# Performance work log

Measured on AMD Instinct MI355X. Metric: run time of the kernel, lower is better.

The kernel has to match this reference:

```python
import jax, jax.numpy as jnp
import numpy as np


def _maxpool2(x):
    # 2x2 max pool, stride 2, valid padding (H, W even). x: [B,H,W,C]
    B, H, W, C = x.shape
    return x.reshape(B, H // 2, 2, W // 2, 2, C).max(axis=(2, 4))


def setup_inputs() -> dict:
    key = jax.random.key(0)
    ks = jax.random.split(key, 9)
    B, H, W, C = 8, 64, 64, 512
    cfg, ch = C // 8, C // 2
    std = 0.02
    return {
        "x": jax.random.normal(ks[0], (B, H, W, C), jnp.float32),
        "theta_w": jax.random.normal(ks[1], (C, cfg), jnp.float32) * std,
        "theta_b": jnp.zeros((cfg,), jnp.float32),
        "phi_w": jax.random.normal(ks[2], (C, cfg), jnp.float32) * std,
        "phi_b": jnp.zeros((cfg,), jnp.float32),
        "g_w": jax.random.normal(ks[3], (C, ch), jnp.float32) * std,
        "g_b": jnp.zeros((ch,), jnp.float32),
        "o3_w": jax.random.normal(ks[4], (ch, C), jnp.float32) * std,
        "o3_b": jnp.zeros((C,), jnp.float32),
        # original initializes gamma to 0; use 0.1 so the attention branch contributes
        "gamma": jnp.full((1,), 0.1, jnp.float32),
    }


def reference(x, theta_w, theta_b, phi_w, phi_b, g_w, g_b, o3_w, o3_b, gamma):
    B, H, W, C = x.shape
    cfg = theta_w.shape[1]
    ch = g_w.shape[1]
    hw = H * W
    hwd = (H // 2) * (W // 2)

    theta = jnp.einsum("bhwc,cf->bhwf", x, theta_w) + theta_b          # [B,H,W,cfg]
    phi = _maxpool2(jnp.einsum("bhwc,cf->bhwf", x, phi_w) + phi_b)     # [B,H/2,W/2,cfg]
    g = _maxpool2(jnp.einsum("bhwc,cg->bhwg", x, g_w) + g_b)           # [B,H/2,W/2,ch]

    theta_f = theta.reshape(B, hw, cfg)
    phi_f = phi.reshape(B, hwd, cfg)
    g_f = g.reshape(B, hwd, ch)

    # s[b,i,j] = phi[b,i] . theta[b,j]; softmax over j (last axis, Keras default)
    s = jnp.einsum("bif,bjf->bij", phi_f, theta_f)                     # [B,hwd,hw]
    beta = jax.nn.softmax(s, axis=-1)
    # o = matmul(beta, g, transpose_a=True): o[b,j,c] = sum_i beta[b,i,j] g[b,i,c]
    o = jnp.einsum("bij,bic->bjc", beta, g_f)                          # [B,hw,ch]
    o = o.reshape(B, H, W, ch)
    o = jnp.einsum("bhwg,gc->bhwc", o, o3_w) + o3_b                    # [B,H,W,C]
    return gamma * o + x
```

## Files before the change

### kernel.cpp

```cpp
#include <hip/hip_runtime.h>
#include <cstdint>

typedef short short8 __attribute__((ext_vector_type(8)));
typedef float floatx4 __attribute__((ext_vector_type(4)));

__device__ __forceinline__ unsigned short f2bf(float f) {
    unsigned int u = __builtin_bit_cast(unsigned int, f);
    u += 0x7FFFu + ((u >> 16) & 1u);
    return (unsigned short)(u >> 16);
}
__device__ __forceinline__ float bf2f(unsigned short h) {
    unsigned int u = ((unsigned int)h) << 16;
    return __builtin_bit_cast(float, u);
}

__device__ __forceinline__ void async_copy16(const void* g, void* lds) {
    __builtin_amdgcn_global_load_lds(
        (const __attribute__((address_space(1))) void*)g,
        (__attribute__((address_space(3))) void*)lds, 16, 0, 0);
}

__device__ __forceinline__ int swz(int row, int koff) {
    return koff ^ (((row >> 2) & 3) << 4);
}

template<bool AFP32, int EPI>
__global__ __launch_bounds__(256) void mfma_gemm(
    const void* __restrict__ Avoid, const unsigned short* __restrict__ B,
    void* __restrict__ Cout, const float* __restrict__ bias,
    const float* __restrict__ gamma, const float* __restrict__ resid,
    int lda, int ldb, int ldc, int K)
{
    __shared__ unsigned short As[4096];
    __shared__ unsigned short Bs[4096];

    const int tid = threadIdx.x;
    const int wv = tid >> 6, ln = tid & 63;
    const int r16 = ln & 15, q8 = ln >> 4;
    const int wm = (wv >> 1) * 64, wn = (wv & 1) * 64;
    const int m0 = blockIdx.y * 128, n0 = blockIdx.x * 128;

    floatx4 acc[4][4] = {};

    for (int k0 = 0; k0 < K; k0 += 32) {
        if (AFP32) {
            const float* Af = (const float*)Avoid;
            #pragma unroll
            for (int p = 0; p < 4; ++p) {
                int u = p * 256 + tid;
                int row = u >> 3, c4 = u & 7;
                float4 v = *(const float4*)(Af + (size_t)(m0 + row) * lda + k0 + c4 * 4);
                ushort4 h;
                h.x = f2bf(v.x); h.y = f2bf(v.y); h.z = f2bf(v.z); h.w = f2bf(v.w);
                *(ushort4*)&As[row * 32 + c4 * 4] = h;
            }
            #pragma unroll
            for (int q = 0; q < 2; ++q) {
                int chunk = wv * 2 + q;
                int e = (chunk << 9) + ln * 8;
                int row = e >> 5, col = e & 31;
                async_copy16(B + (size_t)(n0 + row) * ldb + (k0 + col), &Bs[chunk << 9]);
            }
        } else {
            const unsigned short* Ag = (const unsigned short*)Avoid;
            #pragma unroll
            for (int q = 0; q < 2; ++q) {
                int chunk = wv * 2 + q;
                int e = (chunk << 9) + ln * 8;
                int row = e >> 5, col = e & 31;
                async_copy16(Ag + (size_t)(m0 + row) * lda + (k0 + col), &As[chunk << 9]);
                async_copy16(B + (size_t)(n0 + row) * ldb + (k0 + col), &Bs[chunk << 9]);
            }
        }
        __syncthreads();

        short8 af[4], bff[4];
        #pragma unroll
        for (int i = 0; i < 4; ++i) {
            af[i]  = *(const short8*)&As[(wm + i * 16 + r16) * 32 + q8 * 8];
            bff[i] = *(const short8*)&Bs[(wn + i * 16 + r16) * 32 + q8 * 8];
        }
        #pragma unroll
        for (int mi = 0; mi < 4; ++mi)
            #pragma unroll
            for (int ni = 0; ni < 4; ++ni)
                acc[mi][ni] = __builtin_amdgcn_mfma_f32_16x16x32_bf16(
                    af[mi], bff[ni], acc[mi][ni], 0, 0, 0);
        __syncthreads();
    }

    if (EPI == 2) {
        float* C = (float*)Cout;
        const float gm = gamma[0];
        #pragma unroll
        for (int ni = 0; ni < 4; ++ni) {
            const int n = n0 + wn + ni * 16 + r16;
            const float bs = bias[n];
            #pragma unroll
            for (int mi = 0; mi < 4; ++mi)
                #pragma unroll
                for (int r = 0; r < 4; ++r) {
                    int m = m0 + wm + mi * 16 + q8 * 4 + r;
                    C[(size_t)m * ldc + n] = gm * (acc[mi][ni][r] + bs) + resid[(size_t)m * ldc + n];
                }
        }
    } else {
        unsigned short* C = (unsigned short*)Cout;
        #pragma unroll
        for (int ni = 0; ni < 4; ++ni) {
            const int n = n0 + wn + ni * 16 + r16;
            const float bs = bias[n];
            #pragma unroll
            for (int mi = 0; mi < 4; ++mi)
                #pragma unroll
                for (int r = 0; r < 4; ++r) {
                    int m = m0 + wm + mi * 16 + q8 * 4 + r;
                    C[(size_t)m * ldc + n] = f2bf(acc[mi][ni][r] + bs);
                }
        }
    }
}

__global__ __launch_bounds__(256) void phase1_l_kernel(
    const unsigned short* __restrict__ tpgF,
    const unsigned short* __restrict__ phiP,
    float* __restrict__ lbuf)
{
    __shared__ unsigned short th_s[8192];
    __shared__ unsigned short ph_s[4096];
    const int tid = threadIdx.x, wv = tid >> 6, ln = tid & 63;
    const int r16 = ln & 15, q8 = ln >> 4, lsub = ln >> 3, l8 = ln & 7;
    const int jsp = blockIdx.x, i0 = blockIdx.y * 64, b = blockIdx.z;

    #pragma unroll
    for (int q = 0; q < 2; ++q) {
        int chunk = wv * 2 + q, row = chunk * 8 + lsub;
        int so = swz(row, l8 * 8);
        async_copy16(phiP + (size_t)(b * 1024 + i0 + row) * 64 + so, &ph_s[chunk * 512]);
    }

    float colsum[4] = {0.f, 0.f, 0.f, 0.f};
    for (int jc = 0; jc < 8; ++jc) {
        const int j0 = jsp * 1024 + jc * 128;
        __syncthreads();
        #pragma unroll
        for (int q = 0; q < 4; ++q) {
            int chunk = wv * 4 + q, row = chunk * 8 + lsub;
            int so = swz(row, l8 * 8);
            async_copy16(tpgF + (size_t)(b * 4096 + j0 + row) * 384 + so, &th_s[chunk * 512]);
        }
        __syncthreads();

        floatx4 sacc[2][4] = {};
        #pragma unroll
        for (int ks = 0; ks < 2; ++ks) {
            short8 af[2], bf[4];
            #pragma unroll
            for (int mi = 0; mi < 2; ++mi)
                af[mi] = *(const short8*)&th_s[(wv * 32 + mi * 16 + r16) * 64 + swz(r16, ks * 32 + q8 * 8)];
            #pragma unroll
            for (int ni = 0; ni < 4; ++ni)
                bf[ni] = *(const short8*)&ph_s[(ni * 16 + r16) * 64 + swz(r16, ks * 32 + q8 * 8)];
            #pragma unroll
            for (int mi = 0; mi < 2; ++mi)
                #pragma unroll
                for (int ni = 0; ni < 4; ++ni)
                    sacc[mi][ni] = __builtin_amdgcn_mfma_f32_16x16x32_bf16(
                        af[mi], bf[ni], sacc[mi][ni], 0, 0, 0);
        }
        #pragma unroll
        for (int mi = 0; mi < 2; ++mi)
            #pragma unroll
            for (int ni = 0; ni < 4; ++ni)
                #pragma unroll
                for (int r = 0; r < 4; ++r)
                    colsum[ni] += __expf(sacc[mi][ni][r] - 20.f);
    }
    #pragma unroll
    for (int ni = 0; ni < 4; ++ni) {
        float s = colsum[ni];
        s += __shfl_xor(s, 16);
        s += __shfl_xor(s, 32);
        if (q8 == 0) atomicAdd(&lbuf[b * 1024 + i0 + ni * 16 + r16], s);
    }
}

__global__ __launch_bounds__(512) void attn_fused_kernel(
    const unsigned short* __restrict__ tpgF,
    const unsigned short* __restrict__ phiP,
    const unsigned short* __restrict__ gPT,
    unsigned short* __restrict__ o_)
{
    __shared__ unsigned short th_es[8192];
    __shared__ unsigned short ph_s[2][4096];
    __shared__ unsigned short gs[2][16384];

    const int tid = threadIdx.x, wv = tid >> 6, ln = tid & 63;
    const int r16 = ln & 15, q8 = ln >> 4, lsub = ln >> 3, l8 = ln & 7;
    const int j0 = blockIdx.x * 128, b = blockIdx.y;
    const int jh = wv >> 2, it = wv & 3;

    #pragma unroll
    for (int q = 0; q < 2; ++q) {
        int chunk = wv * 2 + q, row = chunk * 8 + lsub;
        async_copy16(tpgF + (size_t)(b * 4096 + j0 + row) * 384 + swz(row, l8 * 8),
                     &th_es[chunk * 512]);
    }
    {
        int row = wv * 8 + lsub;
        async_copy16(phiP + (size_t)(b * 1024 + row) * 64 + swz(row, l8 * 8),
                     &ph_s[0][wv * 512]);
        #pragma unroll
        for (int q = 0; q < 4; ++q) {
            int chunk = wv * 4 + q, c = chunk * 8 + lsub;
            async_copy16(gPT + (size_t)(b * 256 + c) * 1024 + swz(c, l8 * 8),
                         &gs[0][chunk * 512]);
        }
    }
    asm volatile("s_waitcnt vmcnt(5)" ::: "memory");
    __builtin_amdgcn_sched_barrier(0);
    __builtin_amdgcn_s_barrier();
    __builtin_amdgcn_sched_barrier(0);

    short8 thf[4][2];
    #pragma unroll
    for (int mi = 0; mi < 4; ++mi)
        #pragma unroll
        for (int ks = 0; ks < 2; ++ks)
            thf[mi][ks] = *(const short8*)&th_es[(jh * 64 + mi * 16 + r16) * 64
                                                 + swz(r16, ks * 32 + q8 * 8)];
    asm volatile("s_waitcnt lgkmcnt(0)" ::: "memory");
    __builtin_amdgcn_sched_barrier(0);

    floatx4 acc[4][4] = {};

    for (int t = 0; t < 16; ++t) {
        const int buf = t & 1, nbuf = buf ^ 1;
        if (t < 15) {
            const int i0n = (t + 1) * 64;
            int row = wv * 8 + lsub;
            async_copy16(phiP + (size_t)(b * 1024 + i0n + row) * 64 + swz(row, l8 * 8),
                         &ph_s[nbuf][wv * 512]);
            #pragma unroll
            for (int q = 0; q < 4; ++q) {
                int chunk = wv * 4 + q, c = chunk * 8 + lsub;
                async_copy16(gPT + (size_t)(b * 256 + c) * 1024 + i0n + swz(c, l8 * 8),
                             &gs[nbuf][chunk * 512]);
            }
            asm volatile("s_waitcnt vmcnt(5)" ::: "memory");
        } else {
            asm volatile("s_waitcnt vmcnt(0)" ::: "memory");
        }
        __builtin_amdgcn_sched_barrier(0);
        __builtin_amdgcn_s_barrier();
        __builtin_amdgcn_sched_barrier(0);

        floatx4 sacc[4] = {};
        #pragma unroll
        for (int ks = 0; ks < 2; ++ks) {
            short8 pf = *(const short8*)&ph_s[buf][(it * 16 + r16) * 64
                                                   + swz(r16, ks * 32 + q8 * 8)];
            #pragma unroll
            for (int mi = 0; mi < 4; ++mi)
                sacc[mi] = __builtin_amdgcn_mfma_f32_16x16x32_bf16(
                    thf[mi][ks], pf, sacc[mi], 0, 0, 0);
        }
        #pragma unroll
        for (int mi = 0; mi < 4; ++mi)
            #pragma unroll
            for (int r = 0; r < 4; ++r) {
                int j = jh * 64 + mi * 16 + q8 * 4 + r;
                th_es[j * 64 + (((it ^ q8) << 4) | r16)] = f2bf(__expf(sacc[mi][r] - 20.f));
            }
        asm volatile("s_waitcnt lgkmcnt(0)" ::: "memory");
        __builtin_amdgcn_sched_barrier(0);
        __builtin_amdgcn_s_barrier();
        __builtin_amdgcn_sched_barrier(0);

        #pragma unroll
        for (int ks = 0; ks < 2; ++ks) {
            short8 ef[4], gf[4];
            #pragma unroll
            for (int mi = 0; mi < 4; ++mi)
                ef[mi] = *(const short8*)&th_es[(jh * 64 + mi * 16 + r16) * 64
                                                + swz(r16, ks * 32 + q8 * 8)];
            #pragma unroll
            for (int ni = 0; ni < 4; ++ni)
                gf[ni] = *(const short8*)&gs[buf][(it * 64 + ni * 16 + r16) * 64
                                                  + swz(r16, ks * 32 + q8 * 8)];
            #pragma unroll
            for (int mi = 0; mi < 4; ++mi)
                #pragma unroll
                for (int ni = 0; ni < 4; ++ni)
                    acc[mi][ni] = __builtin_amdgcn_mfma_f32_16x16x32_bf16(
                        ef[mi], gf[ni], acc[mi][ni], 0, 0, 0);
        }
        asm volatile("s_waitcnt lgkmcnt(0)" ::: "memory");
        __builtin_amdgcn_sched_barrier(0);
        __builtin_amdgcn_s_barrier();
        __builtin_amdgcn_sched_barrier(0);
    }

    #pragma unroll
    for (int mi = 0; mi < 4; ++mi)
        #pragma unroll
        for (int ni = 0; ni < 4; ++ni)
            #pragma unroll
            for (int r = 0; r < 4; ++r) {
                int j = j0 + jh * 64 + mi * 16 + q8 * 4 + r;
                int c = it * 64 + ni * 16 + r16;
                o_[((size_t)b * 4096 + j) * 256 + c] = f2bf(acc[mi][ni][r]);
            }
}

__global__ __launch_bounds__(256) void prep_w_kernel(
    const float* __restrict__ theta_w, const float* __restrict__ phi_w,
    const float* __restrict__ g_w, const float* __restrict__ o3_w,
    const float* __restrict__ theta_b, const float* __restrict__ phi_b,
    const float* __restrict__ g_b,
    unsigned short* __restrict__ tpgwT, unsigned short* __restrict__ o3wT,
    float* __restrict__ biasTPG, float* __restrict__ lbuf)
{
    int t = blockIdx.x * 256 + threadIdx.x;
    if (t < 196608) {
        int n = t >> 9, k = t & 511;
        float v = (n < 64) ? theta_w[k * 64 + n]
                : (n < 128) ? phi_w[k * 64 + (n - 64)]
                : g_w[k * 256 + (n - 128)];
        tpgwT[t] = f2bf(v);
    } else if (t < 327680) {
        int e = t - 196608; int n = e >> 8, k = e & 255;
        o3wT[e] = f2bf(o3_w[k * 512 + n]);
    } else if (t < 328064) {
        int j = t - 327680;
        biasTPG[j] = (j < 64) ? theta_b[j] : (j < 128) ? phi_b[j - 64] : g_b[j - 128];
    } else if (t < 336256) {
        lbuf[t - 328064] = 0.f;
    }
}

__global__ __launch_bounds__(256) void maxpool_phi_kernel(
    const unsigned short* __restrict__ tpgF, unsigned short* __restrict__ phiP)
{
    int t = blockIdx.x * 256 + threadIdx.x;
    int f = t & 63, i = (t >> 6) & 1023, b = t >> 16;
    int ph = i >> 5, pw = i & 31;
    size_t base = ((size_t)(b * 64 + 2 * ph) * 64 + 2 * pw) * 384 + 64 + f;
    float v0 = bf2f(tpgF[base]),         v1 = bf2f(tpgF[base + 384]);
    float v2 = bf2f(tpgF[base + 24576]), v3 = bf2f(tpgF[base + 24576 + 384]);
    phiP[t] = f2bf(fmaxf(fmaxf(v0, v1), fmaxf(v2, v3)));
}

__global__ __launch_bounds__(256) void maxpoolT_g_kernel(
    const unsigned short* __restrict__ tpgF, const float* __restrict__ lbuf,
    unsigned short* __restrict__ gPT)
{
    __shared__ unsigned short tile[16][256];
    __shared__ float rls[16];
    int b = blockIdx.y, i0 = blockIdx.x * 16, c = threadIdx.x;
    if (c < 16) rls[c] = 1.0f / lbuf[b * 1024 + i0 + c];
    __syncthreads();
    #pragma unroll
    for (int il = 0; il < 16; ++il) {
        int i = i0 + il, ph = i >> 5, pw = i & 31;
        size_t base = ((size_t)(b * 64 + 2 * ph) * 64 + 2 * pw) * 384 + 128 + c;
        float v0 = bf2f(tpgF[base]),         v1 = bf2f(tpgF[base + 384]);
        float v2 = bf2f(tpgF[base + 24576]), v3 = bf2f(tpgF[base + 24576 + 384]);
        tile[il][c] = f2bf(fmaxf(fmaxf(v0, v1), fmaxf(v2, v3)) * rls[il]);
    }
    __syncthreads();
    unsigned short* dst = gPT + ((size_t)(b * 256 + c) * 1024 + i0);
    short8 v0, v1;
    #pragma unroll
    for (int il = 0; il < 8; ++il) { v0[il] = (short)tile[il][c]; v1[il] = (short)tile[il + 8][c]; }
    *(short8*)dst = v0;
    *(short8*)(dst + 8) = v1;
}

extern "C" void kernel_launch(void* const* d_in, const int* in_sizes, int n_in,
                              void* d_out, int out_size, void* d_ws, size_t ws_size,
                              hipStream_t stream)
{
    const float* x       = (const float*)d_in[0];
    const float* theta_w = (const float*)d_in[1];
    const float* theta_b = (const float*)d_in[2];
    const float* phi_w   = (const float*)d_in[3];
    const float* phi_b   = (const float*)d_in[4];
    const float* g_w     = (const float*)d_in[5];
    const float* g_b     = (const float*)d_in[6];
    const float* o3_w    = (const float*)d_in[7];
    const float* o3_b    = (const float*)d_in[8];
    const float* gamma   = (const float*)d_in[9];

    char* ws = (char*)d_ws;
    unsigned short* tpgwT  = (unsigned short*)(ws);
    unsigned short* o3wT   = (unsigned short*)(ws + 393216);
    float* biasTPG         = (float*)(ws + 655360);
    float* lbuf            = (float*)(ws + 656896);
    unsigned short* tpgF   = (unsigned short*)(ws + (1u << 20));
    unsigned short* phiP   = (unsigned short*)(ws + (1u << 20) + 25165824);
    unsigned short* gPT    = (unsigned short*)(ws + (1u << 20) + 26214400);
    unsigned short* o_     = (unsigned short*)(ws + (1u << 20) + 30408704);

    prep_w_kernel<<<1314, 256, 0, stream>>>(theta_w, phi_w, g_w, o3_w,
                                            theta_b, phi_b, g_b,
                                            tpgwT, o3wT, biasTPG, lbuf);
    mfma_gemm<true, 1><<<dim3(3, 256), 256, 0, stream>>>(
        x, tpgwT, tpgF, biasTPG, nullptr, nullptr, 512, 512, 384, 512);
    maxpool_phi_kernel<<<2048, 256, 0, stream>>>(tpgF, phiP);
    phase1_l_kernel<<<dim3(4, 16, 8), 256, 0, stream>>>(tpgF, phiP, lbuf);
    maxpoolT_g_kernel<<<dim3(64, 8), 256, 0, stream>>>(tpgF, lbuf, gPT);
    attn_fused_kernel<<<dim3(32, 8), 512, 0, stream>>>(tpgF, phiP, gPT, o_);
    mfma_gemm<false, 2><<<dim3(4, 256), 256, 0, stream>>>(
        o_, o3wT, d_out, o3_b, gamma, x, 256, 256, 512, 256);
}
```

Before: 233.1 us.

## Rewrite projection GEMMs with full-N tiles and double-buffered swizzled LDS pipeline

Replaces the 128x128 GEMM with a 512-thread kernel in which each block covers all N columns for its 128 rows. The input activations (fp32 x, or the bf16 attention output) are now read and converted to bf16 only once, instead of once per N-tile. It adds double-buffered LDS with register prefetch of A and async DMA of B, XOR-swizzled LDS layouts, and raised MFMA priority so loads overlap compute. The cost is much larger LDS use per block (about 130KB for the first GEMM), which reduces occupancy, and there are only 256 blocks per launch.

Measured after the change: 226.2 us. -2.9%, faster.

```diff
diff --git a/kernel.cpp b/kernel.cpp
--- a/kernel.cpp
+++ b/kernel.cpp
@@ -24,97 +24,163 @@
     return koff ^ (((row >> 2) & 3) << 4);
 }
 
-template<bool AFP32, int EPI>
-__global__ __launch_bounds__(256) void mfma_gemm(
+template<bool AFP32, int EPI, int BN, int BK, int NT>
+__global__ __launch_bounds__(512, 2) void gemm_nf(
     const void* __restrict__ Avoid, const unsigned short* __restrict__ B,
     void* __restrict__ Cout, const float* __restrict__ bias,
-    const float* __restrict__ gamma, const float* __restrict__ resid,
-    int lda, int ldb, int ldc, int K)
-{
-    __shared__ unsigned short As[4096];
-    __shared__ unsigned short Bs[4096];
+    const float* __restrict__ gammap, const float* __restrict__ resid,
+    int lda, int ldb, int ldc)
+{
+    constexpr int NI = BN / 64;
+    constexpr int KS = BK / 32;
+    constexpr int SLOTM = BK / 16 - 1;
+    constexpr int NB = BN * BK / 4096;
+    constexpr int NPI = NB + (AFP32 ? BK / 16 : BK / 32);
+
+    __shared__ unsigned short As[2][128 * BK];
+    __shared__ unsigned short Bs[2][BN * BK];
 
     const int tid = threadIdx.x;
     const int wv = tid >> 6, ln = tid & 63;
     const int r16 = ln & 15, q8 = ln >> 4;
-    const int wm = (wv >> 1) * 64, wn = (wv & 1) * 64;
-    const int m0 = blockIdx.y * 128, n0 = blockIdx.x * 128;
-
-    floatx4 acc[4][4] = {};
-
-    for (int k0 = 0; k0 < K; k0 += 32) {
-        if (AFP32) {
-            const float* Af = (const float*)Avoid;
-            #pragma unroll
-            for (int p = 0; p < 4; ++p) {
-                int u = p * 256 + tid;
-                int row = u >> 3, c4 = u & 7;
-                float4 v = *(const float4*)(Af + (size_t)(m0 + row) * lda + k0 + c4 * 4);
-                ushort4 h;
-                h.x = f2bf(v.x); h.y = f2bf(v.y); h.z = f2bf(v.z); h.w = f2bf(v.w);
-                *(ushort4*)&As[row * 32 + c4 * 4] = h;
-            }
-            #pragma unroll
-            for (int q = 0; q < 2; ++q) {
-                int chunk = wv * 2 + q;
-                int e = (chunk << 9) + ln * 8;
-                int row = e >> 5, col = e & 31;
-                async_copy16(B + (size_t)(n0 + row) * ldb + (k0 + col), &Bs[chunk << 9]);
-            }
+    const int wr = wv >> 2, wc = wv & 3;
+    const int m0 = blockIdx.x * 128;
+
+    const float* Af = (const float*)Avoid;
+    const unsigned short* Ag = (const unsigned short*)Avoid;
+
+    auto swzT = [](int row, int koff) { return koff ^ (((row >> 2) & SLOTM) << 4); };
+
+    float4 areg[AFP32 ? BK / 16 : 1];
+
+    auto stageB = [&](int t, int sb) {
+        const int k0 = t * BK;
+        #pragma unroll
+        for (int q = 0; q < NB; ++q) {
+            int c = wv * NB + q;
+            if (BK == 64) {
+                int row = c * 8 + (ln >> 3), l8 = ln & 7;
+                async_copy16(B + (size_t)row * ldb + k0 + swzT(row, l8 * 8),
+                             &Bs[sb][c * 512]);
+            } else {
+                int row = c * 16 + (ln >> 2), sl = ln & 3;
+                async_copy16(B + (size_t)row * ldb + k0 + swzT(row, sl * 8),
+                             &Bs[sb][c * 512]);
+            }
+        }
+    };
+    auto stageA_dma = [&](int t, int sb) {
+        const int k0 = t * BK;
+        int row = wv * 16 + (ln >> 2), sl = ln & 3;
+        async_copy16(Ag + (size_t)(m0 + row) * lda + k0 + swzT(row, sl * 8),
+                     &As[sb][wv * 512]);
+    };
+    auto loadA_reg = [&](int t) {
+        const int k0 = t * BK;
+        #pragma unroll
+        for (int p = 0; p < BK / 16; ++p) {
+            int idx = p * 512 + tid;
+            int row = idx >> 4, c4 = idx & 15;
+            areg[p] = *(const float4*)(Af + (size_t)(m0 + row) * lda + k0 + c4 * 4);
+        }
+    };
+    auto writeA = [&](int sb) {
+        #pragma unroll
+        for (int p = 0; p < BK / 16; ++p) {
+            int idx = p * 512 + tid;
+            int row = idx >> 4, c4 = idx & 15;
+            ushort4 h;
+            h.x = f2bf(areg[p].x); h.y = f2bf(areg[p].y);
+            h.z = f2bf(areg[p].z); h.w = f2bf(areg[p].w);
+            *(ushort4*)&As[sb][row * BK + swzT(row, c4 * 4)] = h;
+        }
+    };
+
+    if (AFP32) loadA_reg(0); else stageA_dma(0, 0);
+    stageB(0, 0);
+    if (AFP32) {
+        asm volatile("s_waitcnt vmcnt(%0)" :: "i"(NB) : "memory");
+        __builtin_amdgcn_sched_barrier(0);
+        writeA(0);
+        asm volatile("s_waitcnt lgkmcnt(0)" ::: "memory");
+        __builtin_amdgcn_sched_barrier(0);
+    }
+
+    floatx4 acc[4][NI] = {};
+
+    for (int t = 0; t < NT; ++t) {
+        const int buf = t & 1, nbuf = buf ^ 1;
+        if (t < NT - 1) {
+            if (AFP32) loadA_reg(t + 1); else stageA_dma(t + 1, nbuf);
+            stageB(t + 1, nbuf);
+            asm volatile("s_waitcnt vmcnt(%0)" :: "i"(NPI) : "memory");
         } else {
-            const unsigned short* Ag = (const unsigned short*)Avoid;
-            #pragma unroll
-            for (int q = 0; q < 2; ++q) {
-                int chunk = wv * 2 + q;
-                int e = (chunk << 9) + ln * 8;
-                int row = e >> 5, col = e & 31;
-                async_copy16(Ag + (size_t)(m0 + row) * lda + (k0 + col), &As[chunk << 9]);
-                async_copy16(B + (size_t)(n0 + row) * ldb + (k0 + col), &Bs[chunk << 9]);
-            }
-        }
-        __syncthreads();
-
-        short8 af[4], bff[4];
-        #pragma unroll
-        for (int i = 0; i < 4; ++i) {
-            af[i]  = *(const short8*)&As[(wm + i * 16 + r16) * 32 + q8 * 8];
-            bff[i] = *(const short8*)&Bs[(wn + i * 16 + r16) * 32 + q8 * 8];
-        }
-        #pragma unroll
-        for (int mi = 0; mi < 4; ++mi)
-            #pragma unroll
-            for (int ni = 0; ni < 4; ++ni)
-                acc[mi][ni] = __builtin_amdgcn_mfma_f32_16x16x32_bf16(
-                    af[mi], bff[ni], acc[mi][ni], 0, 0, 0);
-        __syncthreads();
+            asm volatile("s_waitcnt vmcnt(0)" ::: "memory");
+        }
+        __builtin_amdgcn_sched_barrier(0);
+        __builtin_amdgcn_s_barrier();
+        __builtin_amdgcn_sched_barrier(0);
+
+        #pragma unroll
+        for (int ks = 0; ks < KS; ++ks) {
+            short8 af[4], bf[NI];
+            #pragma unroll
+            for (int mi = 0; mi < 4; ++mi) {
+                int row = wr * 64 + mi * 16 + r16;
+                af[mi] = *(const short8*)&As[buf][row * BK + swzT(row, ks * 32 + q8 * 8)];
+            }
+            #pragma unroll
+            for (int ni = 0; ni < NI; ++ni) {
+                int n = wc * (BN / 4) + ni * 16 + r16;
+                bf[ni] = *(const short8*)&Bs[buf][n * BK + swzT(n, ks * 32 + q8 * 8)];
+            }
+            __builtin_amdgcn_s_setprio(1);
+            #pragma unroll
+            for (int mi = 0; mi < 4; ++mi)
+                #pragma unroll
+                for (int ni = 0; ni < NI; ++ni)
+                    acc[mi][ni] = __builtin_amdgcn_mfma_f32_16x16x32_bf16(
+                        af[mi], bf[ni], acc[mi][ni], 0, 0, 0);
+            __builtin_amdgcn_s_setprio(0);
+        }
+
+        if (AFP32 && t < NT - 1) {
+            asm volatile("s_waitcnt vmcnt(%0)" :: "i"(NB) : "memory");
+            __builtin_amdgcn_sched_barrier(0);
+            writeA(nbuf);
+        }
+        asm volatile("s_waitcnt lgkmcnt(0)" ::: "memory");
+        __builtin_amdgcn_sched_barrier(0);
+        __builtin_amdgcn_s_barrier();
+        __builtin_amdgcn_sched_barrier(0);
     }
 
     if (EPI == 2) {
         float* C = (float*)Cout;
-        const float gm = gamma[0];
-        #pragma unroll
-        for (int ni = 0; ni < 4; ++ni) {
-            const int n = n0 + wn + ni * 16 + r16;
+        const float gm = gammap[0];
+        #pragma unroll
+        for (int ni = 0; ni < NI; ++ni) {
+            const int n = wc * (BN / 4) + ni * 16 + r16;
             const float bs = bias[n];
             #pragma unroll
             for (int mi = 0; mi < 4; ++mi)
                 #pragma unroll
                 for (int r = 0; r < 4; ++r) {
-                    int m = m0 + wm + mi * 16 + q8 * 4 + r;
+                    int m = m0 + wr * 64 + mi * 16 + q8 * 4 + r;
                     C[(size_t)m * ldc + n] = gm * (acc[mi][ni][r] + bs) + resid[(size_t)m * ldc + n];
                 }
         }
     } else {
         unsigned short* C = (unsigned short*)Cout;
         #pragma unroll
-        for (int ni = 0; ni < 4; ++ni) {
-            const int n = n0 + wn + ni * 16 + r16;
+        for (int ni = 0; ni < NI; ++ni) {
+            const int n = wc * (BN / 4) + ni * 16 + r16;
             const float bs = bias[n];
             #pragma unroll
             for (int mi = 0; mi < 4; ++mi)
                 #pragma unroll
                 for (int r = 0; r < 4; ++r) {
-                    int m = m0 + wm + mi * 16 + q8 * 4 + r;
+                    int m = m0 + wr * 64 + mi * 16 + q8 * 4 + r;
                     C[(size_t)m * ldc + n] = f2bf(acc[mi][ni][r] + bs);
                 }
         }
@@ -405,12 +471,12 @@
     prep_w_kernel<<<1314, 256, 0, stream>>>(theta_w, phi_w, g_w, o3_w,
                                             theta_b, phi_b, g_b,
                                             tpgwT, o3wT, biasTPG, lbuf);
-    mfma_gemm<true, 1><<<dim3(3, 256), 256, 0, stream>>>(
-        x, tpgwT, tpgF, biasTPG, nullptr, nullptr, 512, 512, 384, 512);
+    gemm_nf<true, 1, 384, 64, 8><<<256, 512, 0, stream>>>(
+        x, tpgwT, tpgF, biasTPG, nullptr, nullptr, 512, 512, 384);
     maxpool_phi_kernel<<<2048, 256, 0, stream>>>(tpgF, phiP);
     phase1_l_kernel<<<dim3(4, 16, 8), 256, 0, stream>>>(tpgF, phiP, lbuf);
     maxpoolT_g_kernel<<<dim3(64, 8), 256, 0, stream>>>(tpgF, lbuf, gPT);
     attn_fused_kernel<<<dim3(32, 8), 512, 0, stream>>>(tpgF, phiP, gPT, o_);
-    mfma_gemm<false, 2><<<dim3(4, 256), 256, 0, stream>>>(
-        o_, o3wT, d_out, o3_b, gamma, x, 256, 256, 512, 256);
-}
+    gemm_nf<false, 2, 512, 32, 8><<<256, 512, 0, stream>>>(
+        o_, o3wT, d_out, o3_b, gamma, x, 256, 256, 512);
+}
```

## Software-pipeline attention scores one tile ahead and swap GEMM grid order

Applied to the files above, without the earlier changes.

The fused attention kernel now computes exp(scores) for tile t+1 into a second LDS buffer while running the PV MFMAs on tile t. This cuts the per-iteration barriers from three to one, and phi is prefetched two tiles ahead in a 4-deep ring. MFMA sections get raised wave priority via s_setprio. Separately, both projection GEMMs swap grid axes so consecutive blocks walk along M rather than N, which changes L2 reuse of the weight and activation tiles. The cost is more LDS per block and higher register pressure from keeping both stages live.

After: 227.0 us. 2.6% less time.

```diff
diff --git a/kernel.cpp b/kernel.cpp
--- a/kernel.cpp
+++ b/kernel.cpp
@@ -38,7 +38,7 @@
     const int wv = tid >> 6, ln = tid & 63;
     const int r16 = ln & 15, q8 = ln >> 4;
     const int wm = (wv >> 1) * 64, wn = (wv & 1) * 64;
-    const int m0 = blockIdx.y * 128, n0 = blockIdx.x * 128;
+    const int m0 = blockIdx.x * 128, n0 = blockIdx.y * 128;
 
     floatx4 acc[4][4] = {};
 
@@ -191,8 +191,9 @@
     const unsigned short* __restrict__ gPT,
     unsigned short* __restrict__ o_)
 {
-    __shared__ unsigned short th_es[8192];
-    __shared__ unsigned short ph_s[2][4096];
+    __shared__ unsigned short es0[8192];
+    __shared__ unsigned short es1[8192];
+    __shared__ unsigned short ph_s[4][4096];
     __shared__ unsigned short gs[2][16384];
 
     const int tid = threadIdx.x, wv = tid >> 6, ln = tid & 63;
@@ -204,11 +205,11 @@
     for (int q = 0; q < 2; ++q) {
         int chunk = wv * 2 + q, row = chunk * 8 + lsub;
         async_copy16(tpgF + (size_t)(b * 4096 + j0 + row) * 384 + swz(row, l8 * 8),
-                     &th_es[chunk * 512]);
+                     &es1[chunk * 512]);
     }
     {
-        int row = wv * 8 + lsub;
-        async_copy16(phiP + (size_t)(b * 1024 + row) * 64 + swz(row, l8 * 8),
+        int prow = wv * 8 + lsub;
+        async_copy16(phiP + (size_t)(b * 1024 + prow) * 64 + swz(prow, l8 * 8),
                      &ph_s[0][wv * 512]);
         #pragma unroll
         for (int q = 0; q < 4; ++q) {
@@ -216,6 +217,8 @@
             async_copy16(gPT + (size_t)(b * 256 + c) * 1024 + swz(c, l8 * 8),
                          &gs[0][chunk * 512]);
         }
+        async_copy16(phiP + (size_t)(b * 1024 + 64 + prow) * 64 + swz(prow, l8 * 8),
+                     &ph_s[1][wv * 512]);
     }
     asm volatile("s_waitcnt vmcnt(5)" ::: "memory");
     __builtin_amdgcn_sched_barrier(0);
@@ -227,78 +230,104 @@
     for (int mi = 0; mi < 4; ++mi)
         #pragma unroll
         for (int ks = 0; ks < 2; ++ks)
-            thf[mi][ks] = *(const short8*)&th_es[(jh * 64 + mi * 16 + r16) * 64
+            thf[mi][ks] = *(const short8*)&es1[(jh * 64 + mi * 16 + r16) * 64
+                                               + swz(r16, ks * 32 + q8 * 8)];
+
+    {
+        floatx4 sacc[4] = {};
+        #pragma unroll
+        for (int ks = 0; ks < 2; ++ks) {
+            short8 pf = *(const short8*)&ph_s[0][(it * 16 + r16) * 64
                                                  + swz(r16, ks * 32 + q8 * 8)];
-    asm volatile("s_waitcnt lgkmcnt(0)" ::: "memory");
+            #pragma unroll
+            for (int mi = 0; mi < 4; ++mi)
+                sacc[mi] = __builtin_amdgcn_mfma_f32_16x16x32_bf16(
+                    thf[mi][ks], pf, sacc[mi], 0, 0, 0);
+        }
+        #pragma unroll
+        for (int mi = 0; mi < 4; ++mi)
+            #pragma unroll
+            for (int r = 0; r < 4; ++r) {
+                int j = jh * 64 + mi * 16 + q8 * 4 + r;
+                es0[j * 64 + (((it ^ q8) << 4) | r16)] = f2bf(__expf(sacc[mi][r] - 20.f));
+            }
+    }
+    asm volatile("s_waitcnt vmcnt(0) lgkmcnt(0)" ::: "memory");
+    __builtin_amdgcn_sched_barrier(0);
+    __builtin_amdgcn_s_barrier();
     __builtin_amdgcn_sched_barrier(0);
 
     floatx4 acc[4][4] = {};
 
     for (int t = 0; t < 16; ++t) {
         const int buf = t & 1, nbuf = buf ^ 1;
+        unsigned short* esr = buf ? es1 : es0;
+        unsigned short* esw = buf ? es0 : es1;
+        const unsigned short* gsr = gs[buf];
+        unsigned short* gsw = gs[nbuf];
+
         if (t < 15) {
-            const int i0n = (t + 1) * 64;
-            int row = wv * 8 + lsub;
-            async_copy16(phiP + (size_t)(b * 1024 + i0n + row) * 64 + swz(row, l8 * 8),
-                         &ph_s[nbuf][wv * 512]);
             #pragma unroll
             for (int q = 0; q < 4; ++q) {
                 int chunk = wv * 4 + q, c = chunk * 8 + lsub;
-                async_copy16(gPT + (size_t)(b * 256 + c) * 1024 + i0n + swz(c, l8 * 8),
-                             &gs[nbuf][chunk * 512]);
-            }
-            asm volatile("s_waitcnt vmcnt(5)" ::: "memory");
-        } else {
-            asm volatile("s_waitcnt vmcnt(0)" ::: "memory");
-        }
-        __builtin_amdgcn_sched_barrier(0);
-        __builtin_amdgcn_s_barrier();
-        __builtin_amdgcn_sched_barrier(0);
-
-        floatx4 sacc[4] = {};
-        #pragma unroll
-        for (int ks = 0; ks < 2; ++ks) {
-            short8 pf = *(const short8*)&ph_s[buf][(it * 16 + r16) * 64
-                                                   + swz(r16, ks * 32 + q8 * 8)];
-            #pragma unroll
-            for (int mi = 0; mi < 4; ++mi)
-                sacc[mi] = __builtin_amdgcn_mfma_f32_16x16x32_bf16(
-                    thf[mi][ks], pf, sacc[mi], 0, 0, 0);
-        }
-        #pragma unroll
-        for (int mi = 0; mi < 4; ++mi)
-            #pragma unroll
-            for (int r = 0; r < 4; ++r) {
-                int j = jh * 64 + mi * 16 + q8 * 4 + r;
-                th_es[j * 64 + (((it ^ q8) << 4) | r16)] = f2bf(__expf(sacc[mi][r] - 20.f));
-            }
-        asm volatile("s_waitcnt lgkmcnt(0)" ::: "memory");
-        __builtin_amdgcn_sched_barrier(0);
-        __builtin_amdgcn_s_barrier();
-        __builtin_amdgcn_sched_barrier(0);
+                async_copy16(gPT + (size_t)(b * 256 + c) * 1024 + (t + 1) * 64 + swz(c, l8 * 8),
+                             &gsw[chunk * 512]);
+            }
+        }
+        if (t < 14) {
+            int prow = wv * 8 + lsub;
+            async_copy16(phiP + (size_t)(b * 1024 + (t + 2) * 64 + prow) * 64 + swz(prow, l8 * 8),
+                         &ph_s[(t + 2) & 3][wv * 512]);
+        }
+
+        if (t < 15) {
+            const unsigned short* php = ph_s[(t + 1) & 3];
+            floatx4 sacc[4] = {};
+            #pragma unroll
+            for (int ks = 0; ks < 2; ++ks) {
+                short8 pf = *(const short8*)&php[(it * 16 + r16) * 64
+                                                 + swz(r16, ks * 32 + q8 * 8)];
+                #pragma unroll
+                for (int mi = 0; mi < 4; ++mi)
+                    sacc[mi] = __builtin_amdgcn_mfma_f32_16x16x32_bf16(
+                        thf[mi][ks], pf, sacc[mi], 0, 0, 0);
+            }
+            #pragma unroll
+            for (int mi = 0; mi < 4; ++mi)
+                #pragma unroll
+                for (int r = 0; r < 4; ++r) {
+                    int j = jh * 64 + mi * 16 + q8 * 4 + r;
+                    esw[j * 64 + (((it ^ q8) << 4) | r16)] = f2bf(__expf(sacc[mi][r] - 20.f));
+                }
+        }
 
         #pragma unroll
         for (int ks = 0; ks < 2; ++ks) {
             short8 ef[4], gf[4];
             #pragma unroll
             for (int mi = 0; mi < 4; ++mi)
-                ef[mi] = *(const short8*)&th_es[(jh * 64 + mi * 16 + r16) * 64
-                                                + swz(r16, ks * 32 + q8 * 8)];
+                ef[mi] = *(const short8*)&esr[(jh * 64 + mi * 16 + r16) * 64
+                                              + swz(r16, ks * 32 + q8 * 8)];
             #pragma unroll
             for (int ni = 0; ni < 4; ++ni)
-                gf[ni] = *(const short8*)&gs[buf][(it * 64 + ni * 16 + r16) * 64
-                                                  + swz(r16, ks * 32 + q8 * 8)];
+                gf[ni] = *(const short8*)&gsr[(it * 64 + ni * 16 + r16) * 64
+                                              + swz(r16, ks * 32 + q8 * 8)];
+            __builtin_amdgcn_s_setprio(1);
             #pragma unroll
             for (int mi = 0; mi < 4; ++mi)
                 #pragma unroll
                 for (int ni = 0; ni < 4; ++ni)
                     acc[mi][ni] = __builtin_amdgcn_mfma_f32_16x16x32_bf16(
                         ef[mi], gf[ni], acc[mi][ni], 0, 0, 0);
-        }
-        asm volatile("s_waitcnt lgkmcnt(0)" ::: "memory");
-        __builtin_amdgcn_sched_barrier(0);
-        __builtin_amdgcn_s_barrier();
-        __builtin_amdgcn_sched_barrier(0);
+            __builtin_amdgcn_s_setprio(0);
+        }
+
+        if (t < 15) {
+            asm volatile("s_waitcnt vmcnt(0) lgkmcnt(0)" ::: "memory");
+            __builtin_amdgcn_sched_barrier(0);
+            __builtin_amdgcn_s_barrier();
+            __builtin_amdgcn_sched_barrier(0);
+        }
     }
 
     #pragma unroll
@@ -405,12 +434,12 @@
     prep_w_kernel<<<1314, 256, 0, stream>>>(theta_w, phi_w, g_w, o3_w,
                                             theta_b, phi_b, g_b,
                                             tpgwT, o3wT, biasTPG, lbuf);
-    mfma_gemm<true, 1><<<dim3(3, 256), 256, 0, stream>>>(
+    mfma_gemm<true, 1><<<dim3(256, 3), 256, 0, stream>>>(
         x, tpgwT, tpgF, biasTPG, nullptr, nullptr, 512, 512, 384, 512);
     maxpool_phi_kernel<<<2048, 256, 0, stream>>>(tpgF, phiP);
     phase1_l_kernel<<<dim3(4, 16, 8), 256, 0, stream>>>(tpgF, phiP, lbuf);
     maxpoolT_g_kernel<<<dim3(64, 8), 256, 0, stream>>>(tpgF, lbuf, gPT);
     attn_fused_kernel<<<dim3(32, 8), 512, 0, stream>>>(tpgF, phiP, gPT, o_);
-    mfma_gemm<false, 2><<<dim3(4, 256), 256, 0, stream>>>(
+    mfma_gemm<false, 2><<<dim3(256, 4), 256, 0, stream>>>(
         o_, o3wT, d_out, o3_b, gamma, x, 256, 256, 512, 256);
 }
```

## Drop LDS staging in phase1 softmax-denominator kernel, load theta directly to registers

Applied to the files above, without the earlier changes.

The phase1 kernel that computes the softmax row sums no longer stages theta and phi tiles through shared memory with async copies and barriers. Each wave keeps its own 16 phi rows in registers and streams theta rows straight from global memory into MFMA operands. The grid doubles along j, so each block covers 512 columns instead of 1024. This removes LDS traffic and __syncthreads stalls, but gives up reuse of theta across the four waves, so the same theta data is read up to four times from global memory or cache.

Result: slower. 252.2 us (+8.2%).

```diff
diff --git a/kernel.cpp b/kernel.cpp
--- a/kernel.cpp
+++ b/kernel.cpp
@@ -126,63 +126,34 @@
     const unsigned short* __restrict__ phiP,
     float* __restrict__ lbuf)
 {
-    __shared__ unsigned short th_s[8192];
-    __shared__ unsigned short ph_s[4096];
     const int tid = threadIdx.x, wv = tid >> 6, ln = tid & 63;
-    const int r16 = ln & 15, q8 = ln >> 4, lsub = ln >> 3, l8 = ln & 7;
+    const int r16 = ln & 15, q8 = ln >> 4;
     const int jsp = blockIdx.x, i0 = blockIdx.y * 64, b = blockIdx.z;
-
-    #pragma unroll
-    for (int q = 0; q < 2; ++q) {
-        int chunk = wv * 2 + q, row = chunk * 8 + lsub;
-        int so = swz(row, l8 * 8);
-        async_copy16(phiP + (size_t)(b * 1024 + i0 + row) * 64 + so, &ph_s[chunk * 512]);
-    }
-
-    float colsum[4] = {0.f, 0.f, 0.f, 0.f};
-    for (int jc = 0; jc < 8; ++jc) {
-        const int j0 = jsp * 1024 + jc * 128;
-        __syncthreads();
-        #pragma unroll
-        for (int q = 0; q < 4; ++q) {
-            int chunk = wv * 4 + q, row = chunk * 8 + lsub;
-            int so = swz(row, l8 * 8);
-            async_copy16(tpgF + (size_t)(b * 4096 + j0 + row) * 384 + so, &th_s[chunk * 512]);
-        }
-        __syncthreads();
-
-        floatx4 sacc[2][4] = {};
-        #pragma unroll
-        for (int ks = 0; ks < 2; ++ks) {
-            short8 af[2], bf[4];
-            #pragma unroll
-            for (int mi = 0; mi < 2; ++mi)
-                af[mi] = *(const short8*)&th_s[(wv * 32 + mi * 16 + r16) * 64 + swz(r16, ks * 32 + q8 * 8)];
-            #pragma unroll
-            for (int ni = 0; ni < 4; ++ni)
-                bf[ni] = *(const short8*)&ph_s[(ni * 16 + r16) * 64 + swz(r16, ks * 32 + q8 * 8)];
-            #pragma unroll
-            for (int mi = 0; mi < 2; ++mi)
-                #pragma unroll
-                for (int ni = 0; ni < 4; ++ni)
-                    sacc[mi][ni] = __builtin_amdgcn_mfma_f32_16x16x32_bf16(
-                        af[mi], bf[ni], sacc[mi][ni], 0, 0, 0);
-        }
-        #pragma unroll
-        for (int mi = 0; mi < 2; ++mi)
-            #pragma unroll
-            for (int ni = 0; ni < 4; ++ni)
-                #pragma unroll
-                for (int r = 0; r < 4; ++r)
-                    colsum[ni] += __expf(sacc[mi][ni][r] - 20.f);
-    }
-    #pragma unroll
-    for (int ni = 0; ni < 4; ++ni) {
-        float s = colsum[ni];
-        s += __shfl_xor(s, 16);
-        s += __shfl_xor(s, 32);
-        if (q8 == 0) atomicAdd(&lbuf[b * 1024 + i0 + ni * 16 + r16], s);
-    }
+    const int iw = i0 + wv * 16;
+
+    short8 bf[2];
+    #pragma unroll
+    for (int ks = 0; ks < 2; ++ks)
+        bf[ks] = *(const short8*)&phiP[(size_t)(b * 1024 + iw + r16) * 64 + ks * 32 + q8 * 8];
+
+    const unsigned short* th = tpgF + (size_t)(b * 4096 + jsp * 512) * 384 + q8 * 8;
+
+    float colsum = 0.f;
+    #pragma unroll 4
+    for (int jc = 0; jc < 32; ++jc) {
+        const unsigned short* tr = th + (size_t)(jc * 16 + r16) * 384;
+        short8 a0 = *(const short8*)tr;
+        short8 a1 = *(const short8*)(tr + 32);
+        floatx4 sacc = {};
+        sacc = __builtin_amdgcn_mfma_f32_16x16x32_bf16(a0, bf[0], sacc, 0, 0, 0);
+        sacc = __builtin_amdgcn_mfma_f32_16x16x32_bf16(a1, bf[1], sacc, 0, 0, 0);
+        #pragma unroll
+        for (int r = 0; r < 4; ++r)
+            colsum += __expf(sacc[r] - 20.f);
+    }
+    colsum += __shfl_xor(colsum, 16);
+    colsum += __shfl_xor(colsum, 32);
+    if (q8 == 0) atomicAdd(&lbuf[b * 1024 + iw + r16], colsum);
 }
 
 __global__ __launch_bounds__(512) void attn_fused_kernel(
@@ -408,7 +379,7 @@
     mfma_gemm<true, 1><<<dim3(3, 256), 256, 0, stream>>>(
         x, tpgwT, tpgF, biasTPG, nullptr, nullptr, 512, 512, 384, 512);
     maxpool_phi_kernel<<<2048, 256, 0, stream>>>(tpgF, phiP);
-    phase1_l_kernel<<<dim3(4, 16, 8), 256, 0, stream>>>(tpgF, phiP, lbuf);
+    phase1_l_kernel<<<dim3(8, 16, 8), 256, 0, stream>>>(tpgF, phiP, lbuf);
     maxpoolT_g_kernel<<<dim3(64, 8), 256, 0, stream>>>(tpgF, lbuf, gPT);
     attn_fused_kernel<<<dim3(32, 8), 512, 0, stream>>>(tpgF, phiP, gPT, o_);
     mfma_gemm<false, 2><<<dim3(4, 256), 256, 0, stream>>>(
```
